# Kernel optimization log

Measured on AMD Instinct MI355X. Metric: run time of the kernel, lower is better.

## Reference

```python
import jax, jax.numpy as jnp
import numpy as np

N_BINS = 64
INPUT_DIM = 8
R = 1.2
BOUND = 10.0
BETA = 1e-06
N = 2097152


def _mesh_and_elmt():
    m = N_BINS / 2
    idx = jnp.arange(N_BINS + 1, dtype=jnp.float32) - m
    x1L = BOUND * (R - 1.0) / (R ** m - 1.0)
    xr = (1.0 - R ** jnp.abs(idx)) / (1.0 - R)
    xr = jnp.where(idx >= 0, x1L * xr, -x1L * xr)
    xr = (xr + BOUND) / (2.0 * BOUND)
    mesh = jnp.concatenate([jnp.zeros((1,), jnp.float32), xr[1:-1], jnp.ones((1,), jnp.float32)])  # [n_bins+1]
    elmt = mesh[1:] - mesh[:-1]  # [n_bins]
    return mesh, elmt


def _pdf_normalize(p, elmt):
    # pdf: [n_bins+1, d]; F_ref: [n_bins, d] cumulative bin integrals
    p0 = jnp.full((1, INPUT_DIM), BETA, jnp.float32)
    ep = jnp.exp(p)
    px = ep * ((elmt[:-1] + elmt[1:]) / 2.0)[:, None]
    scale = (1.0 - (elmt[0] + elmt[-1]) * BETA / 2.0) / jnp.sum(px, 0, keepdims=True)
    px = scale * ep
    pdf = jnp.concatenate([p0, px, p0], 0)
    cell = (pdf[:-1] + pdf[1:]) / 2.0 * elmt[:, None]  # [n_bins, d]
    F_ref = jnp.concatenate([jnp.zeros((1, INPUT_DIM), jnp.float32),
                             jnp.cumsum(cell, 0)[:N_BINS - 1]], 0)
    return pdf, F_ref


def setup_inputs() -> dict:
    key = jax.random.key(0)
    k1, k2 = jax.random.split(key)
    x = jax.random.normal(k1, (N, INPUT_DIM), dtype=jnp.float32)
    logdet = jnp.zeros((N, 1), dtype=jnp.float32)
    p = jax.random.normal(k2, (N_BINS - 1, INPUT_DIM), dtype=jnp.float32)
    return {"x": x, "logdet": logdet, "p": p}


def reference(x, logdet, p):
    mesh, elmt = _mesh_and_elmt()
    pdf, F_ref = _pdf_normalize(p, elmt)

    xs = (x + BOUND) / (2.0 * BOUND)  # [N, d] in [0,1] for covered points
    k = jnp.searchsorted(mesh, xs, side='right') - 1  # [N, d]
    cover = (k >= 0) & (k <= N_BINS - 1)
    k = jnp.clip(k, 0, N_BINS - 1)
    col = jnp.arange(INPUT_DIM)[None, :]

    v1 = pdf[k, col]            # [N, d]
    v2 = pdf[k + 1, col]
    xm = xs - mesh[k]
    h = elmt[k]
    F_pre = F_ref[k, col]

    y = jnp.where(cover, F_pre + xm * xm / 2.0 * (v2 - v1) / h + xm * v1, xs)
    dld = jnp.where(cover, xm * (v2 - v1) / h + v1, 1.0)
    logdet = logdet + jnp.sum(jnp.log(dld), -1, keepdims=True)

    y = y * 2.0 * BOUND - BOUND
    y = jnp.where(y > BOUND, BETA * (y - BOUND) + BOUND, y)
    logdet = logdet + jnp.sum(jnp.log(jnp.where(y > BOUND, BETA, 1.0)), -1, keepdims=True)
    y = jnp.where(y < -BOUND, BETA * (y + BOUND) - BOUND, y)
    logdet = logdet + jnp.sum(jnp.log(jnp.where(y < -BOUND, BETA, 1.0)), -1, keepdims=True)
    return y, logdet
```

## Files before the change

### kernel.cpp

```cpp
#include <hip/hip_runtime.h>
#include <hip/hip_bf16.h>
#include <math.h>

#define NDIM   8
#define NBINS  64
#define LOG_BETA   (-13.815510557964274f)
#define LN2F       0.69314718055994531f
#define ALPHA      34.0821892f
#define INV_LOG2R  3.80178401692393f

__global__ __launch_bounds__(256, 8) void cdfq_fused(const float* __restrict__ x,
                                                     const float* __restrict__ logdet_in,
                                                     const float* __restrict__ p,
                                                     float* __restrict__ y_out,
                                                     float* __restrict__ ld_out,
                                                     int n)
{
    __shared__ float  mesh[65];
    __shared__ float  elmt[64];
    __shared__ float  sc[NDIM];
    __shared__ float  pdfs[NDIM][65];
    __shared__ float4 stbl[NDIM * NBINS];

    const int t  = threadIdx.x;
    const int T  = gridDim.x * blockDim.x;
    const int i0 = blockIdx.x * blockDim.x + t;
    const int G  = 2 * n;
    const int iters = G / T;
    const float4* xv4 = (const float4*)x;

    float4 Xc; float Lc;
    if (iters > 0) {
        Xc = xv4[i0];
        Lc = logdet_in[i0 >> 1];
    }
    __builtin_amdgcn_sched_barrier(0);

    if (t < 65) {
        float fidx = (float)t - 32.0f;
        float a = fabsf(fidx);
        float x1L = 2.0f / (powf(1.2f, 32.0f) - 1.0f);
        float xr = x1L * (powf(1.2f, a) - 1.0f) / 0.2f;
        xr = (fidx >= 0.0f) ? xr : -xr;
        xr = (xr + 10.0f) / 20.0f;
        if (t == 0)  xr = 0.0f;
        if (t == 64) xr = 1.0f;
        mesh[t] = xr;
    }
    for (int idx = t; idx < 63 * NDIM; idx += 256) {
        int d = idx & 7, k = idx >> 3;
        pdfs[d][k + 1] = expf(p[k * NDIM + d]);
    }
    if (t < NDIM) { pdfs[t][0] = 1e-6f; pdfs[t][64] = 1e-6f; }
    __syncthreads();
    if (t < 64) elmt[t] = mesh[t + 1] - mesh[t];
    __syncthreads();

    if (t < 64) {
        for (int d = 0; d < NDIM; ++d) {
            float w = 0.0f;
            if (t < 63) w = pdfs[d][t + 1] * 0.5f * (elmt[t] + elmt[t + 1]);
            for (int off = 32; off > 0; off >>= 1) w += __shfl_down(w, off);
            if (t == 0) sc[d] = (1.0f - (elmt[0] + elmt[63]) * 5e-7f) / w;
        }
    }
    __syncthreads();
    for (int idx = t; idx < 63 * NDIM; idx += 256) {
        int d = idx & 7, k = idx >> 3;
        pdfs[d][k + 1] *= sc[d];
    }
    __syncthreads();
    if (t < 64) {
        for (int d = 0; d < NDIM; ++d) {
            float c0 = 0.5f * (pdfs[d][t] + pdfs[d][t + 1]) * elmt[t];
            float v = c0;
            for (int off = 1; off < 64; off <<= 1) {
                float w = __shfl_up(v, off);
                if (t >= off) v += w;
            }
            float Fpre = v - c0;
            float v1 = pdfs[d][t];
            float v2 = pdfs[d][t + 1];
            stbl[d * 64 + t] = make_float4(v1, (v2 - v1) / elmt[t], Fpre, mesh[t]);
        }
    }
    __syncthreads();

    auto body = [&](float4 X, float Lin, int g) {
        const int q     = g >> 1;
        const int dbase = (g & 1) << 2;
        float xd[4] = {X.x, X.y, X.z, X.w};
        float yd[4], dd[4];
        float extra = 0.0f;

#pragma unroll
        for (int dl = 0; dl < 4; ++dl) {
            float xo = xd[dl];
            float xs = fmaf(xo, 0.05f, 0.5f);
            float u  = fabsf(xo);
            float gg = __log2f(fmaf(ALPHA, u, 1.0f)) * INV_LOG2R;
            int jp = (int)fminf(gg, 31.0f);
            int jn = (int)ceilf(fminf(gg, 32.0f));
            int k  = (xo >= 0.0f) ? (32 + jp) : (32 - jn);

            float4 tb = stbl[((dbase + dl) << 6) + k];
            float xm  = xs - tb.w;
            bool cov  = (xs >= 0.0f) && (xs < 1.0f);

            float yc = tb.z + xm * fmaf(0.5f * xm, tb.y, tb.x);
            float dv = fmaf(xm, tb.y, tb.x);
            float yy = cov ? yc : xs;
            dd[dl]   = cov ? dv : 1.0f;

            yy = fmaf(yy, 20.0f, -10.0f);
            if (yy > 10.0f)  { yy = fmaf(1e-6f, yy - 10.0f, 10.0f);  extra += LOG_BETA; }
            if (yy < -10.0f) { yy = fmaf(1e-6f, yy + 10.0f, -10.0f); extra += LOG_BETA; }
            yd[dl] = yy;
        }

        float l2 = __log2f(dd[0] * dd[1]) + __log2f(dd[2] * dd[3]);
        float contrib = fmaf(l2, LN2F, extra);
        float cross   = __shfl_xor(contrib, 1);

        ((float4*)y_out)[g] = make_float4(yd[0], yd[1], yd[2], yd[3]);
        if ((g & 1) == 0) ld_out[q] = Lin + contrib + cross;
    };

    for (int j = 0; j < iters; ++j) {
        float4 Xn; float Ln;
        const bool more = (j + 1 < iters);
        if (more) {
            int gx = i0 + (j + 1) * T;
            Xn = xv4[gx];
            Ln = logdet_in[gx >> 1];
        }
        __builtin_amdgcn_sched_barrier(0);

        body(Xc, Lc, i0 + j * T);

        if (more) { Xc = Xn; Lc = Ln; }
    }

    int gr = i0 + iters * T;
    if (gr < G) {
        body(xv4[gr], logdet_in[gr >> 1], gr);
    }
}

extern "C" void kernel_launch(void* const* d_in, const int* in_sizes, int n_in,
                              void* d_out, int out_size, void* d_ws, size_t ws_size,
                              hipStream_t stream) {
    const float* x      = (const float*)d_in[0];
    const float* logdet = (const float*)d_in[1];
    const float* p      = (const float*)d_in[2];

    const int n = in_sizes[1];
    float* y_out  = (float*)d_out;
    float* ld_out = (float*)d_out + (size_t)n * NDIM;

    const int block = 256;
    int grid = 2048;
    if ((long long)grid * block > 2LL * n) grid = (2 * n + block - 1) / block;
    cdfq_fused<<<grid, block, 0, stream>>>(x, logdet, p, y_out, ld_out, n);
}
```

Baseline: 138.5 us.

## Deepen prefetch to two iterations, streamline table setup, use nontemporal stores

The main loop now keeps two iterations of input loads in flight instead of one, so more memory latency is hidden. The per-block table setup is rewritten to compute mesh and element widths in registers and to do the normalization and prefix scans per wave with shuffles. This drops the shared staging arrays and most of the barriers. Output stores become nontemporal to avoid polluting the cache, and the bin index computation is simplified. The cost is extra registers from the second prefetch buffer, and the changed index formula could differ at bin edges.

Measured after the change: 136.3 us. About the same (-1.6%).

```diff
diff --git a/kernel.cpp b/kernel.cpp
--- a/kernel.cpp
+++ b/kernel.cpp
@@ -1,5 +1,4 @@
 #include <hip/hip_runtime.h>
-#include <hip/hip_bf16.h>
 #include <math.h>
 
 #define NDIM   8
@@ -8,6 +7,9 @@
 #define LN2F       0.69314718055994531f
 #define ALPHA      34.0821892f
 #define INV_LOG2R  3.80178401692393f
+#define L2R        0.26303440583379378f
+
+typedef float f32x4 __attribute__((ext_vector_type(4)));
 
 __global__ __launch_bounds__(256, 8) void cdfq_fused(const float* __restrict__ x,
                                                      const float* __restrict__ logdet_in,
@@ -16,10 +18,6 @@
                                                      float* __restrict__ ld_out,
                                                      int n)
 {
-    __shared__ float  mesh[65];
-    __shared__ float  elmt[64];
-    __shared__ float  sc[NDIM];
-    __shared__ float  pdfs[NDIM][65];
     __shared__ float4 stbl[NDIM * NBINS];
 
     const int t  = threadIdx.x;
@@ -29,59 +27,48 @@
     const int iters = G / T;
     const float4* xv4 = (const float4*)x;
 
-    float4 Xc; float Lc;
-    if (iters > 0) {
-        Xc = xv4[i0];
-        Lc = logdet_in[i0 >> 1];
-    }
+    float4 X0, X1; float L0, L1;
+    if (iters > 0) { X0 = xv4[i0];     L0 = logdet_in[i0 >> 1]; }
+    if (iters > 1) { X1 = xv4[i0 + T]; L1 = logdet_in[(i0 + T) >> 1]; }
     __builtin_amdgcn_sched_barrier(0);
 
-    if (t < 65) {
-        float fidx = (float)t - 32.0f;
-        float a = fabsf(fidx);
-        float x1L = 2.0f / (powf(1.2f, 32.0f) - 1.0f);
-        float xr = x1L * (powf(1.2f, a) - 1.0f) / 0.2f;
-        xr = (fidx >= 0.0f) ? xr : -xr;
-        xr = (xr + 10.0f) / 20.0f;
-        if (t == 0)  xr = 0.0f;
-        if (t == 64) xr = 1.0f;
-        mesh[t] = xr;
-    }
-    for (int idx = t; idx < 63 * NDIM; idx += 256) {
-        int d = idx & 7, k = idx >> 3;
-        pdfs[d][k + 1] = expf(p[k * NDIM + d]);
-    }
-    if (t < NDIM) { pdfs[t][0] = 1e-6f; pdfs[t][64] = 1e-6f; }
-    __syncthreads();
-    if (t < 64) elmt[t] = mesh[t + 1] - mesh[t];
-    __syncthreads();
+    {
+        const int lane = t & 63;
+        const int w    = t >> 6;
+        const float pw32 = exp2f(32.0f * L2R);
+        const float inv  = 0.5f / (pw32 - 1.0f);
+        auto meshf = [&](float tt) {
+            float fidx = tt - 32.0f;
+            float pw = exp2f(fabsf(fidx) * L2R);
+            float r  = (pw - 1.0f) * inv;
+            return 0.5f + ((fidx >= 0.0f) ? r : -r);
+        };
+        const float m0  = meshf((float)lane);
+        const float m1  = meshf((float)(lane + 1));
+        const float el  = m1 - m0;
+        const float el1 = __shfl_down(el, 1);
+        const float e0e63 = 2.0f * (meshf(1.0f) - meshf(0.0f));
 
-    if (t < 64) {
-        for (int d = 0; d < NDIM; ++d) {
-            float w = 0.0f;
-            if (t < 63) w = pdfs[d][t + 1] * 0.5f * (elmt[t] + elmt[t + 1]);
-            for (int off = 32; off > 0; off >>= 1) w += __shfl_down(w, off);
-            if (t == 0) sc[d] = (1.0f - (elmt[0] + elmt[63]) * 5e-7f) / w;
-        }
-    }
-    __syncthreads();
-    for (int idx = t; idx < 63 * NDIM; idx += 256) {
-        int d = idx & 7, k = idx >> 3;
-        pdfs[d][k + 1] *= sc[d];
-    }
-    __syncthreads();
-    if (t < 64) {
-        for (int d = 0; d < NDIM; ++d) {
-            float c0 = 0.5f * (pdfs[d][t] + pdfs[d][t + 1]) * elmt[t];
-            float v = c0;
+#pragma unroll
+        for (int dd = 0; dd < 2; ++dd) {
+            const int d = 2 * w + dd;
+            float ep = 0.0f;
+            if (lane < 63) ep = __expf(p[lane * NDIM + d]);
+            float s = ep * 0.5f * (el + el1);
+#pragma unroll
+            for (int off = 32; off; off >>= 1) s += __shfl_xor(s, off);
+            const float scale = (1.0f - e0e63 * 5e-7f) / s;
+            const float epu = __shfl_up(ep, 1);
+            const float pdl = (lane == 0)  ? 1e-6f : scale * epu;
+            const float pdn = (lane == 63) ? 1e-6f : scale * ep;
+            const float cell = 0.5f * (pdl + pdn) * el;
+            float v = cell;
+#pragma unroll
             for (int off = 1; off < 64; off <<= 1) {
-                float w = __shfl_up(v, off);
-                if (t >= off) v += w;
+                float u = __shfl_up(v, off);
+                if (lane >= off) v += u;
             }
-            float Fpre = v - c0;
-            float v1 = pdfs[d][t];
-            float v2 = pdfs[d][t + 1];
-            stbl[d * 64 + t] = make_float4(v1, (v2 - v1) / elmt[t], Fpre, mesh[t]);
+            stbl[(d << 6) | lane] = make_float4(pdl, (pdn - pdl) / el, v - cell, m0);
         }
     }
     __syncthreads();
@@ -90,18 +77,16 @@
         const int q     = g >> 1;
         const int dbase = (g & 1) << 2;
         float xd[4] = {X.x, X.y, X.z, X.w};
-        float yd[4], dd[4];
+        float yd[4], dd4[4];
         float extra = 0.0f;
 
 #pragma unroll
         for (int dl = 0; dl < 4; ++dl) {
             float xo = xd[dl];
             float xs = fmaf(xo, 0.05f, 0.5f);
-            float u  = fabsf(xo);
-            float gg = __log2f(fmaf(ALPHA, u, 1.0f)) * INV_LOG2R;
-            int jp = (int)fminf(gg, 31.0f);
-            int jn = (int)ceilf(fminf(gg, 32.0f));
-            int k  = (xo >= 0.0f) ? (32 + jp) : (32 - jn);
+            float gg = __log2f(fmaf(ALPHA, fabsf(xo), 1.0f)) * INV_LOG2R;
+            int jf = (int)fminf(gg, 31.0f);
+            int k  = (xo >= 0.0f) ? (32 + jf) : (31 - jf);
 
             float4 tb = stbl[((dbase + dl) << 6) + k];
             float xm  = xs - tb.w;
@@ -110,7 +95,7 @@
             float yc = tb.z + xm * fmaf(0.5f * xm, tb.y, tb.x);
             float dv = fmaf(xm, tb.y, tb.x);
             float yy = cov ? yc : xs;
-            dd[dl]   = cov ? dv : 1.0f;
+            dd4[dl]  = cov ? dv : 1.0f;
 
             yy = fmaf(yy, 20.0f, -10.0f);
             if (yy > 10.0f)  { yy = fmaf(1e-6f, yy - 10.0f, 10.0f);  extra += LOG_BETA; }
@@ -118,27 +103,30 @@
             yd[dl] = yy;
         }
 
-        float l2 = __log2f(dd[0] * dd[1]) + __log2f(dd[2] * dd[3]);
+        float l2 = __log2f(dd4[0] * dd4[1]) + __log2f(dd4[2] * dd4[3]);
         float contrib = fmaf(l2, LN2F, extra);
         float cross   = __shfl_xor(contrib, 1);
 
-        ((float4*)y_out)[g] = make_float4(yd[0], yd[1], yd[2], yd[3]);
-        if ((g & 1) == 0) ld_out[q] = Lin + contrib + cross;
+        f32x4 yv = { yd[0], yd[1], yd[2], yd[3] };
+        __builtin_nontemporal_store(yv, (f32x4*)y_out + g);
+        if ((g & 1) == 0)
+            __builtin_nontemporal_store(Lin + contrib + cross, ld_out + q);
     };
 
     for (int j = 0; j < iters; ++j) {
         float4 Xn; float Ln;
-        const bool more = (j + 1 < iters);
+        const bool more = (j + 2 < iters);
         if (more) {
-            int gx = i0 + (j + 1) * T;
+            int gx = i0 + (j + 2) * T;
             Xn = xv4[gx];
             Ln = logdet_in[gx >> 1];
         }
         __builtin_amdgcn_sched_barrier(0);
 
-        body(Xc, Lc, i0 + j * T);
+        body(X0, L0, i0 + j * T);
 
-        if (more) { Xc = Xn; Lc = Ln; }
+        X0 = X1; L0 = L1;
+        if (more) { X1 = Xn; L1 = Ln; }
     }
 
     int gr = i0 + iters * T;
```
